# Performance work log

Measured on AMD Instinct MI355X. Metric: run time of the kernel, lower is better.

## Reference

```python
import jax, jax.numpy as jnp
import numpy as np

N_NODES = 50000
N_EDGES = 800000
IN_C = 64
OUT_C = 64
K = 4  # spectral coefficients; weight has K+1 slices (selfconn)
EPS = 1e-16  # PyG segment-softmax epsilon


def setup_inputs() -> dict:
    key = jax.random.key(0)
    k1, k2, k3, k4, k5 = jax.random.split(key, 5)
    x = jax.random.normal(k1, (N_NODES, IN_C), dtype=jnp.float32)
    edge_index = jax.random.randint(k2, (2, N_EDGES), 0, N_NODES, dtype=jnp.int64)
    edge_attr = jax.random.normal(k3, (N_EDGES, K), dtype=jnp.float32)
    # glorot-style scale for weight [K+1, in, out]
    stdv = np.sqrt(6.0 / (IN_C + OUT_C))
    weight = jax.random.uniform(k4, (K + 1, IN_C, OUT_C), dtype=jnp.float32,
                                minval=-stdv, maxval=stdv)
    bias = jnp.zeros((OUT_C,), dtype=jnp.float32)
    att_vector = jax.random.normal(k5, (IN_C, 1), dtype=jnp.float32) * 0.1
    return {"x": x, "edge_attr": edge_attr, "weight": weight, "bias": bias,
            "att_vector": att_vector, "edge_index": edge_index}


def _segment_softmax(logits, seg, num_segments):
    mx = jax.ops.segment_max(logits, seg, num_segments=num_segments)
    ex = jnp.exp(logits - mx[seg])
    den = jax.ops.segment_sum(ex, seg, num_segments=num_segments)
    return ex / (den[seg] + EPS)


def reference(x, edge_attr, weight, bias, att_vector, edge_index):
    src, dst = edge_index[0], edge_index[1]
    n_nodes = x.shape[0]
    # messages for all K coefficients at once: [E, K, C]
    msgs = edge_attr[:, :, None] * x[src][:, None, :]
    # sum branch: per-k scatter_add then per-k weight -> fused einsum
    sum_agg = jax.ops.segment_sum(msgs, dst, num_segments=n_nodes)  # [N, K, C]
    sum_out = x @ weight[-1] + jnp.einsum('nkc,kco->no', sum_agg, weight[:K])
    # attention branch
    pooled = msgs.mean(axis=1)                       # [E, C]
    raw_att = (pooled @ att_vector)[:, 0]            # [E]
    att_scores = _segment_softmax(raw_att, dst, n_nodes)
    att_agg = jax.ops.segment_sum(att_scores[:, None, None] * msgs, dst,
                                  num_segments=n_nodes)  # [N, K, C]
    out = sum_out + jnp.einsum('nkc,kco->no', att_agg, weight[:K]) + bias
    return out, att_scores
```

## Files before the change

kernel.cpp:

```cpp
#include <hip/hip_runtime.h>
#include <math.h>

#define C 64
#define KCOEF 4
#define FN 128
#define FK 64
#define APAD 65

#define BSH 6
#define RN 64
#define CAP 1280
#define EPB 4
#define MAXNBK 1024

__global__ __launch_bounds__(256) void kAH(const float* __restrict__ x,
        const float* __restrict__ attv, const int* __restrict__ dst,
        float* __restrict__ dvec, int* __restrict__ deg, int N, int E, int NBD) {
    if ((int)blockIdx.x < NBD) {
        int t = threadIdx.x;
        int n = blockIdx.x * 16 + (t >> 4);
        int q = t & 15;
        if (n >= N) return;
        float4 xv = *(const float4*)(x + (size_t)n * C + q * 4);
        float4 av = *(const float4*)(attv + q * 4);
        float p = xv.x * av.x + xv.y * av.y + xv.z * av.z + xv.w * av.w;
        #pragma unroll
        for (int o = 8; o > 0; o >>= 1) p += __shfl_xor(p, o, 16);
        if (q == 0) dvec[n] = p;
    } else {
        int e = ((int)blockIdx.x - NBD) * 256 + (int)threadIdx.x;
        if (e >= E) return;
        atomicAdd(&deg[dst[e]], 1);
    }
}

__global__ __launch_bounds__(256) void kS1(const int* __restrict__ deg,
        int* __restrict__ off, int* __restrict__ bsum, int N) {
    int g = blockIdx.x * 256 + threadIdx.x;
    int lane = threadIdx.x & 63, w = threadIdx.x >> 6;
    int v = (g < N) ? deg[g] : 0;
    int incl = v;
    #pragma unroll
    for (int s = 1; s < 64; s <<= 1) {
        int t = __shfl_up(incl, s);
        if (lane >= s) incl += t;
    }
    __shared__ int wtot[4];
    if (lane == 63) wtot[w] = incl;
    __syncthreads();
    int add = 0;
    for (int ww = 0; ww < w; ++ww) add += wtot[ww];
    int excl = incl - v + add;
    if (g < N) off[g] = excl;
    if (threadIdx.x == 255) bsum[blockIdx.x] = excl + v;
}

__global__ __launch_bounds__(256) void kS2(int* __restrict__ bsum, int NB) {
    int t = threadIdx.x;
    int lane = t & 63, w = t >> 6;
    int v = (t < NB) ? bsum[t] : 0;
    int incl = v;
    #pragma unroll
    for (int s = 1; s < 64; s <<= 1) {
        int tt = __shfl_up(incl, s);
        if (lane >= s) incl += tt;
    }
    __shared__ int wtot[4];
    if (lane == 63) wtot[w] = incl;
    __syncthreads();
    int add = 0;
    for (int ww = 0; ww < w; ++ww) add += wtot[ww];
    if (t < NB) bsum[t] = incl - v + add;
}

__global__ __launch_bounds__(256) void kS3(int* __restrict__ off,
        const int* __restrict__ bsum, int* __restrict__ gcur, int N, int E) {
    int g = blockIdx.x * 256 + threadIdx.x;
    if (g == 0) off[N] = E;
    if (g >= N) return;
    int o = off[g] + bsum[blockIdx.x];
    off[g] = o;
    if ((g & (RN - 1)) == 0) gcur[g >> BSH] = o;
}

__global__ __launch_bounds__(1024) void kBIN(const int* __restrict__ src,
        const int* __restrict__ dst, const float* __restrict__ ea,
        const float* __restrict__ dvec, int* __restrict__ gcur,
        float4* __restrict__ pay, int E, int NBK) {
    __shared__ int hist[MAXNBK];
    __shared__ int cursor[MAXNBK];
    int tid = threadIdx.x;
    int base = blockIdx.x * (1024 * EPB);
    for (int b = tid; b < NBK; b += 1024) hist[b] = 0;
    __syncthreads();
    #pragma unroll
    for (int i = 0; i < EPB; ++i) {
        int e = base + i * 1024 + tid;
        if (e < E) atomicAdd(&hist[dst[e] >> BSH], 1);
    }
    __syncthreads();
    for (int b = tid; b < NBK; b += 1024) cursor[b] = atomicAdd(&gcur[b], hist[b]);
    __syncthreads();
    #pragma unroll
    for (int i = 0; i < EPB; ++i) {
        int e = base + i * 1024 + tid;
        if (e < E) {
            int sN = src[e];
            int d  = dst[e];
            float4 a = ((const float4*)ea)[e];
            float mean = (a.x + a.y + a.z + a.w) * 0.25f;
            float r = mean * dvec[sN];
            int p = atomicAdd(&cursor[d >> BSH], 1);
            int xo = ((d & (RN - 1)) << 24) | (sN << 8);
            float4 q0 = make_float4(r, __int_as_float(xo), a.x, a.y);
            float4 q1 = make_float4(a.z, a.w, 0.f, 0.f);
            pay[(size_t)p * 2]     = q0;
            pay[(size_t)p * 2 + 1] = q1;
        }
    }
}

__global__ __launch_bounds__(512) void kAGG(const float* __restrict__ x,
        const float4* __restrict__ pay, const int* __restrict__ off,
        float* __restrict__ mA, float* __restrict__ invA,
        float* __restrict__ agg, int N) {
    __shared__ float  rA[CAP];
    __shared__ int    xoA[CAP];
    __shared__ float4 qA[CAP];
    __shared__ int    no[RN + 1];
    __shared__ int    ncur[RN];
    __shared__ float  mL[RN], ivL[RN];
    int tid = threadIdx.x;
    int n0 = (int)blockIdx.x << BSH;
    int n1 = min(n0 + RN, N);
    int nn = n1 - n0;
    int bstart = off[n0];
    int cnt = off[n1] - bstart;
    if (cnt > CAP) cnt = CAP;
    if (tid <= nn) {
        int o = off[n0 + tid] - bstart;
        o = min(o, CAP);
        no[tid] = o;
        if (tid < nn) ncur[tid] = o;
    }
    __syncthreads();
    for (int i = tid; i < cnt; i += 512) {
        float4 p0 = pay[(size_t)(bstart + i) * 2];
        float4 p1 = pay[(size_t)(bstart + i) * 2 + 1];
        int v = __float_as_int(p0.y);
        int p = atomicAdd(&ncur[v >> 24], 1);
        rA[p]  = p0.x;
        xoA[p] = v;
        qA[p]  = make_float4(p0.z, p0.w, p1.x, p1.y);
    }
    __syncthreads();
    int wv = tid >> 6, lane = tid & 63;
    for (int nl = wv; nl < nn; nl += 8) {
        int s = no[nl];
        int d = no[nl + 1] - s;
        int n = n0 + nl;
        if (d == 0) {
            if (lane == 0) { mL[nl] = 0.f; ivL[nl] = 1.f; mA[n] = 0.f; invA[n] = 1.f; }
            continue;
        }
        float m = -INFINITY;
        for (int i = lane; i < d; i += 64) m = fmaxf(m, rA[s + i]);
        #pragma unroll
        for (int o = 32; o > 0; o >>= 1) m = fmaxf(m, __shfl_xor(m, o));
        float ss = 0.f;
        for (int i = lane; i < d; i += 64) ss += expf(rA[s + i] - m);
        #pragma unroll
        for (int o = 32; o > 0; o >>= 1) ss += __shfl_xor(ss, o);
        float inv = 1.f / (ss + 1e-16f);
        if (lane == 0) { mL[nl] = m; ivL[nl] = inv; mA[n] = m; invA[n] = inv; }
    }
    __syncthreads();
    for (int i = tid; i < cnt; i += 512) {
        int dl = xoA[i] >> 24;
        rA[i] = 1.f + expf(rA[i] - mL[dl]) * ivL[dl];
    }
    __syncthreads();
    const char* xb = (const char*)x + (size_t)lane * 4;
    for (int nl = wv; nl < nn; nl += 8) {
        int s = no[nl];
        int d = no[nl + 1] - s;
        int n = n0 + nl;
        size_t ab = (size_t)n * (KCOEF * C) + lane;
        float a0 = 0.f, a1 = 0.f, a2 = 0.f, a3 = 0.f;
        #pragma unroll 4
        for (int j = 0; j < d; ++j) {
            float w = rA[s + j];
            float4 q = qA[s + j];
            int ob = xoA[s + j] & 0xFFFFFF;
            float xr = *(const float*)(xb + ob);
            float wx = w * xr;
            a0 = fmaf(q.x, wx, a0);
            a1 = fmaf(q.y, wx, a1);
            a2 = fmaf(q.z, wx, a2);
            a3 = fmaf(q.w, wx, a3);
        }
        agg[ab] = a0; agg[ab + 64] = a1; agg[ab + 128] = a2; agg[ab + 192] = a3;
    }
}

__global__ __launch_bounds__(256) void kF3(const float* __restrict__ agg,
        const float* __restrict__ x, const float* __restrict__ W,
        const float* __restrict__ bias, float* __restrict__ out_node, int N) {
    __shared__ float As[FN][APAD];
    __shared__ float Ws[FK][C];
    int tid = threadIdx.x;
    int nbase = blockIdx.x * FN;
    int ng = tid >> 3;
    int cg = tid & 7;
    float4 acc0[4], acc1[4];
    #pragma unroll
    for (int j = 0; j < 4; ++j) { acc0[j] = {0,0,0,0}; acc1[j] = {0,0,0,0}; }

    int srow_q = tid & 15;
    int srow_b = tid >> 4;

    for (int k0 = 0; k0 < 320; k0 += FK) {
        #pragma unroll
        for (int pass = 0; pass < 8; ++pass) {
            int row = pass * 16 + srow_b;
            int n = nbase + row; if (n >= N) n = N - 1;
            float4 v;
            if (k0 < 256) v = *(const float4*)(agg + (size_t)n * 256 + k0 + srow_q * 4);
            else          v = *(const float4*)(x   + (size_t)n * C   + srow_q * 4);
            As[row][srow_q * 4 + 0] = v.x;
            As[row][srow_q * 4 + 1] = v.y;
            As[row][srow_q * 4 + 2] = v.z;
            As[row][srow_q * 4 + 3] = v.w;
        }
        #pragma unroll
        for (int p = 0; p < 4; ++p) {
            int idx = tid + p * 256;
            ((float4*)Ws)[idx] = ((const float4*)(W + (size_t)k0 * C))[idx];
        }
        __syncthreads();
        #pragma unroll 2
        for (int i = 0; i < FK; ++i) {
            float a0 = As[ng * 4 + 0][i];
            float a1 = As[ng * 4 + 1][i];
            float a2 = As[ng * 4 + 2][i];
            float a3 = As[ng * 4 + 3][i];
            float4 w0 = *(const float4*)&Ws[i][cg * 8];
            float4 w1 = *(const float4*)&Ws[i][cg * 8 + 4];
            acc0[0].x = fmaf(a0, w0.x, acc0[0].x); acc0[0].y = fmaf(a0, w0.y, acc0[0].y);
            acc0[0].z = fmaf(a0, w0.z, acc0[0].z); acc0[0].w = fmaf(a0, w0.w, acc0[0].w);
            acc1[0].x = fmaf(a0, w1.x, acc1[0].x); acc1[0].y = fmaf(a0, w1.y, acc1[0].y);
            acc1[0].z = fmaf(a0, w1.z, acc1[0].z); acc1[0].w = fmaf(a0, w1.w, acc1[0].w);
            acc0[1].x = fmaf(a1, w0.x, acc0[1].x); acc0[1].y = fmaf(a1, w0.y, acc0[1].y);
            acc0[1].z = fmaf(a1, w0.z, acc0[1].z); acc0[1].w = fmaf(a1, w0.w, acc0[1].w);
            acc1[1].x = fmaf(a1, w1.x, acc1[1].x); acc1[1].y = fmaf(a1, w1.y, acc1[1].y);
            acc1[1].z = fmaf(a1, w1.z, acc1[1].z); acc1[1].w = fmaf(a1, w1.w, acc1[1].w);
            acc0[2].x = fmaf(a2, w0.x, acc0[2].x); acc0[2].y = fmaf(a2, w0.y, acc0[2].y);
            acc0[2].z = fmaf(a2, w0.z, acc0[2].z); acc0[2].w = fmaf(a2, w0.w, acc0[2].w);
            acc1[2].x = fmaf(a2, w1.x, acc1[2].x); acc1[2].y = fmaf(a2, w1.y, acc1[2].y);
            acc1[2].z = fmaf(a2, w1.z, acc1[2].z); acc1[2].w = fmaf(a2, w1.w, acc1[2].w);
            acc0[3].x = fmaf(a3, w0.x, acc0[3].x); acc0[3].y = fmaf(a3, w0.y, acc0[3].y);
            acc0[3].z = fmaf(a3, w0.z, acc0[3].z); acc0[3].w = fmaf(a3, w0.w, acc0[3].w);
            acc1[3].x = fmaf(a3, w1.x, acc1[3].x); acc1[3].y = fmaf(a3, w1.y, acc1[3].y);
            acc1[3].z = fmaf(a3, w1.z, acc1[3].z); acc1[3].w = fmaf(a3, w1.w, acc1[3].w);
        }
        __syncthreads();
    }
    float4 bA = *(const float4*)(bias + cg * 8);
    float4 bB = *(const float4*)(bias + cg * 8 + 4);
    #pragma unroll
    for (int j = 0; j < 4; ++j) {
        int n = nbase + ng * 4 + j;
        if (n < N) {
            float4 oA = { acc0[j].x + bA.x, acc0[j].y + bA.y, acc0[j].z + bA.z, acc0[j].w + bA.w };
            float4 oB = { acc1[j].x + bB.x, acc1[j].y + bB.y, acc1[j].z + bB.z, acc1[j].w + bB.w };
            *(float4*)(out_node + (size_t)n * C + cg * 8)     = oA;
            *(float4*)(out_node + (size_t)n * C + cg * 8 + 4) = oB;
        }
    }
}

__global__ __launch_bounds__(256) void kT(const int* __restrict__ src,
        const int* __restrict__ dst, const float* __restrict__ ea,
        const float* __restrict__ dvec, const float* __restrict__ mA,
        const float* __restrict__ invA, float* __restrict__ out_att, int E) {
    int e = blockIdx.x * 256 + threadIdx.x;
    if (e >= E) return;
    float4 a = ((const float4*)ea)[e];
    float mean = (a.x + a.y + a.z + a.w) * 0.25f;
    float r = mean * dvec[src[e]];
    int d = dst[e];
    out_att[e] = expf(r - mA[d]) * invA[d];
}

extern "C" void kernel_launch(void* const* d_in, const int* in_sizes, int n_in,
                              void* d_out, int out_size, void* d_ws, size_t ws_size,
                              hipStream_t stream) {
    const float* x    = (const float*)d_in[0];
    const float* ea   = (const float*)d_in[1];
    const float* W    = (const float*)d_in[2];
    const float* bias = (const float*)d_in[3];
    const float* attv = (const float*)d_in[4];
    const int*   ei   = (const int*)d_in[5];

    int N = in_sizes[0] / C;
    int E = in_sizes[5] / 2;
    const int* src = ei;
    const int* dst = ei + E;

    float* out_node = (float*)d_out;
    float* out_att  = (float*)d_out + (size_t)N * C;

    char* ws = (char*)d_ws;
    float* agg  = (float*)ws; ws += (size_t)N * KCOEF * C * sizeof(float);
    float4* pay = (float4*)ws; ws += (size_t)E * 32;
    float* dvec = (float*)ws; ws += (size_t)N * sizeof(float);
    int*   deg  = (int*)ws;   ws += (size_t)N * sizeof(int);
    int*   off  = (int*)ws;   ws += (size_t)(N + 1) * sizeof(int);
    float* mA   = (float*)ws; ws += (size_t)N * sizeof(float);
    int*   gcur = (int*)ws;   ws += MAXNBK * sizeof(int);
    int*   bsum = (int*)ws;   ws += 1024;

    float* invA = (float*)deg;

    int NB  = (N + 255) / 256;
    int NBD = (N + 15) / 16;
    int NBH = (E + 255) / 256;
    int NBK = (N + RN - 1) >> BSH;
    int NBB = (E + 1024 * EPB - 1) / (1024 * EPB);
    int NBF = (N + FN - 1) / FN;

    hipMemsetAsync(deg, 0, (size_t)N * sizeof(int), stream);
    kAH  <<<NBD + NBH, 256, 0, stream>>>(x, attv, dst, dvec, deg, N, E, NBD);
    kS1  <<<NB, 256, 0, stream>>>(deg, off, bsum, N);
    kS2  <<<1, 256, 0, stream>>>(bsum, NB);
    kS3  <<<NB, 256, 0, stream>>>(off, bsum, gcur, N, E);
    kBIN <<<NBB, 1024, 0, stream>>>(src, dst, ea, dvec, gcur, pay, E, NBK);
    kAGG <<<NBK, 512, 0, stream>>>(x, pay, off, mA, invA, agg, N);
    kF3  <<<NBF, 256, 0, stream>>>(agg, x, W, bias, out_node, N);
    kT   <<<NBH, 256, 0, stream>>>(src, dst, ea, dvec, mA, invA, out_att, E);
}
```

Baseline: 252.0 us.

## Replace per-node degree scan with per-bucket histogram and in-block node offsets

The per-node degree atomics and the three-kernel prefix scan over N nodes are replaced by a shared-memory histogram per 64-node bucket and a single-block scan over about 800 buckets. Per-node offsets inside each bucket are now rebuilt in the aggregation kernel by counting a new byte array of local destination indices and doing a wave scan. The payload is also split into a 16-byte record and an 8-byte record instead of a padded 32-byte one, which cuts write and read traffic. This removes two launches and the global per-node atomics, but adds a counting pass and an extra byte stream inside kAGG.

```diff
diff --git a/kernel.cpp b/kernel.cpp
--- a/kernel.cpp
+++ b/kernel.cpp
@@ -11,11 +11,13 @@
 #define RN 64
 #define CAP 1280
 #define EPB 4
+#define EH  16
 #define MAXNBK 1024
 
 __global__ __launch_bounds__(256) void kAH(const float* __restrict__ x,
         const float* __restrict__ attv, const int* __restrict__ dst,
-        float* __restrict__ dvec, int* __restrict__ deg, int N, int E, int NBD) {
+        float* __restrict__ dvec, int* __restrict__ bcnt,
+        int N, int E, int NBD, int NBK) {
     if ((int)blockIdx.x < NBD) {
         int t = threadIdx.x;
         int n = blockIdx.x * 16 + (t >> 4);
@@ -28,65 +30,48 @@
         for (int o = 8; o > 0; o >>= 1) p += __shfl_xor(p, o, 16);
         if (q == 0) dvec[n] = p;
     } else {
-        int e = ((int)blockIdx.x - NBD) * 256 + (int)threadIdx.x;
-        if (e >= E) return;
-        atomicAdd(&deg[dst[e]], 1);
-    }
-}
-
-__global__ __launch_bounds__(256) void kS1(const int* __restrict__ deg,
-        int* __restrict__ off, int* __restrict__ bsum, int N) {
-    int g = blockIdx.x * 256 + threadIdx.x;
-    int lane = threadIdx.x & 63, w = threadIdx.x >> 6;
-    int v = (g < N) ? deg[g] : 0;
-    int incl = v;
-    #pragma unroll
-    for (int s = 1; s < 64; s <<= 1) {
-        int t = __shfl_up(incl, s);
-        if (lane >= s) incl += t;
-    }
-    __shared__ int wtot[4];
-    if (lane == 63) wtot[w] = incl;
-    __syncthreads();
-    int add = 0;
-    for (int ww = 0; ww < w; ++ww) add += wtot[ww];
-    int excl = incl - v + add;
-    if (g < N) off[g] = excl;
-    if (threadIdx.x == 255) bsum[blockIdx.x] = excl + v;
-}
-
-__global__ __launch_bounds__(256) void kS2(int* __restrict__ bsum, int NB) {
-    int t = threadIdx.x;
-    int lane = t & 63, w = t >> 6;
-    int v = (t < NB) ? bsum[t] : 0;
+        __shared__ int hist[MAXNBK];
+        int tid = threadIdx.x;
+        for (int b = tid; b < NBK; b += 256) hist[b] = 0;
+        __syncthreads();
+        int base = ((int)blockIdx.x - NBD) * (256 * EH);
+        for (int i = 0; i < EH; ++i) {
+            int e = base + i * 256 + tid;
+            if (e < E) atomicAdd(&hist[dst[e] >> BSH], 1);
+        }
+        __syncthreads();
+        for (int b = tid; b < NBK; b += 256) {
+            int h = hist[b];
+            if (h) atomicAdd(&bcnt[b], h);
+        }
+    }
+}
+
+__global__ __launch_bounds__(1024) void kSB(const int* __restrict__ bcnt,
+        int* __restrict__ base_, int* __restrict__ gcur, int NBK) {
+    int t = threadIdx.x, lane = t & 63, wv = t >> 6;
+    int v = (t < NBK) ? bcnt[t] : 0;
     int incl = v;
     #pragma unroll
     for (int s = 1; s < 64; s <<= 1) {
         int tt = __shfl_up(incl, s);
         if (lane >= s) incl += tt;
     }
-    __shared__ int wtot[4];
-    if (lane == 63) wtot[w] = incl;
+    __shared__ int wtot[16];
+    if (lane == 63) wtot[wv] = incl;
     __syncthreads();
     int add = 0;
-    for (int ww = 0; ww < w; ++ww) add += wtot[ww];
-    if (t < NB) bsum[t] = incl - v + add;
-}
-
-__global__ __launch_bounds__(256) void kS3(int* __restrict__ off,
-        const int* __restrict__ bsum, int* __restrict__ gcur, int N, int E) {
-    int g = blockIdx.x * 256 + threadIdx.x;
-    if (g == 0) off[N] = E;
-    if (g >= N) return;
-    int o = off[g] + bsum[blockIdx.x];
-    off[g] = o;
-    if ((g & (RN - 1)) == 0) gcur[g >> BSH] = o;
+    for (int w = 0; w < wv; ++w) add += wtot[w];
+    int excl = incl - v + add;
+    if (t <= NBK) base_[t] = excl;
+    if (t <  NBK) gcur[t]  = excl;
 }
 
 __global__ __launch_bounds__(1024) void kBIN(const int* __restrict__ src,
         const int* __restrict__ dst, const float* __restrict__ ea,
         const float* __restrict__ dvec, int* __restrict__ gcur,
-        float4* __restrict__ pay, int E, int NBK) {
+        float4* __restrict__ pay16, float2* __restrict__ pay8,
+        unsigned char* __restrict__ dlA, int E, int NBK) {
     __shared__ int hist[MAXNBK];
     __shared__ int cursor[MAXNBK];
     int tid = threadIdx.x;
@@ -99,7 +84,10 @@
         if (e < E) atomicAdd(&hist[dst[e] >> BSH], 1);
     }
     __syncthreads();
-    for (int b = tid; b < NBK; b += 1024) cursor[b] = atomicAdd(&gcur[b], hist[b]);
+    for (int b = tid; b < NBK; b += 1024) {
+        int h = hist[b];
+        cursor[b] = h ? atomicAdd(&gcur[b], h) : 0;
+    }
     __syncthreads();
     #pragma unroll
     for (int i = 0; i < EPB; ++i) {
@@ -110,18 +98,19 @@
             float4 a = ((const float4*)ea)[e];
             float mean = (a.x + a.y + a.z + a.w) * 0.25f;
             float r = mean * dvec[sN];
+            int dl = d & (RN - 1);
             int p = atomicAdd(&cursor[d >> BSH], 1);
-            int xo = ((d & (RN - 1)) << 24) | (sN << 8);
-            float4 q0 = make_float4(r, __int_as_float(xo), a.x, a.y);
-            float4 q1 = make_float4(a.z, a.w, 0.f, 0.f);
-            pay[(size_t)p * 2]     = q0;
-            pay[(size_t)p * 2 + 1] = q1;
+            int xo = (dl << 24) | (sN << 8);
+            pay16[p] = make_float4(r, __int_as_float(xo), a.x, a.y);
+            pay8[p]  = make_float2(a.z, a.w);
+            dlA[p]   = (unsigned char)dl;
         }
     }
 }
 
 __global__ __launch_bounds__(512) void kAGG(const float* __restrict__ x,
-        const float4* __restrict__ pay, const int* __restrict__ off,
+        const float4* __restrict__ pay16, const float2* __restrict__ pay8,
+        const unsigned char* __restrict__ dlA, const int* __restrict__ base_,
         float* __restrict__ mA, float* __restrict__ invA,
         float* __restrict__ agg, int N) {
     __shared__ float  rA[CAP];
@@ -129,24 +118,38 @@
     __shared__ float4 qA[CAP];
     __shared__ int    no[RN + 1];
     __shared__ int    ncur[RN];
+    __shared__ int    ncnt[RN];
     __shared__ float  mL[RN], ivL[RN];
     int tid = threadIdx.x;
-    int n0 = (int)blockIdx.x << BSH;
+    int b = (int)blockIdx.x;
+    int n0 = b << BSH;
     int n1 = min(n0 + RN, N);
     int nn = n1 - n0;
-    int bstart = off[n0];
-    int cnt = off[n1] - bstart;
+    int bstart = base_[b];
+    int cnt = base_[b + 1] - bstart;
     if (cnt > CAP) cnt = CAP;
-    if (tid <= nn) {
-        int o = off[n0 + tid] - bstart;
-        o = min(o, CAP);
-        no[tid] = o;
-        if (tid < nn) ncur[tid] = o;
-    }
+    if (tid < RN) ncnt[tid] = 0;
+    __syncthreads();
+    for (int i = tid; i < cnt; i += 512) atomicAdd(&ncnt[dlA[bstart + i]], 1);
+    __syncthreads();
+    int wv = tid >> 6, lane = tid & 63;
+    if (wv == 0) {
+        int v = (lane < nn) ? ncnt[lane] : 0;
+        int incl = v;
+        #pragma unroll
+        for (int s = 1; s < 64; s <<= 1) {
+            int tt = __shfl_up(incl, s);
+            if (lane >= s) incl += tt;
+        }
+        no[lane + 1] = incl;
+        if (lane == 0) no[0] = 0;
+    }
+    __syncthreads();
+    if (tid < nn) ncur[tid] = no[tid];
     __syncthreads();
     for (int i = tid; i < cnt; i += 512) {
-        float4 p0 = pay[(size_t)(bstart + i) * 2];
-        float4 p1 = pay[(size_t)(bstart + i) * 2 + 1];
+        float4 p0 = pay16[(size_t)bstart + i];
+        float2 p1 = pay8[(size_t)bstart + i];
         int v = __float_as_int(p0.y);
         int p = atomicAdd(&ncur[v >> 24], 1);
         rA[p]  = p0.x;
@@ -154,7 +157,6 @@
         qA[p]  = make_float4(p0.z, p0.w, p1.x, p1.y);
     }
     __syncthreads();
-    int wv = tid >> 6, lane = tid & 63;
     for (int nl = wv; nl < nn; nl += 8) {
         int s = no[nl];
         int d = no[nl + 1] - s;
@@ -311,31 +313,30 @@
     float* out_att  = (float*)d_out + (size_t)N * C;
 
     char* ws = (char*)d_ws;
-    float* agg  = (float*)ws; ws += (size_t)N * KCOEF * C * sizeof(float);
-    float4* pay = (float4*)ws; ws += (size_t)E * 32;
+    float* agg   = (float*)ws; ws += (size_t)N * KCOEF * C * sizeof(float);
+    float4* pay16 = (float4*)ws; ws += (size_t)E * 16;
+    float2* pay8  = (float2*)ws; ws += (size_t)E * 8;
+    unsigned char* dlA = (unsigned char*)ws; ws += (size_t)E;
+    ws = (char*)(((size_t)ws + 255) & ~(size_t)255);
     float* dvec = (float*)ws; ws += (size_t)N * sizeof(float);
-    int*   deg  = (int*)ws;   ws += (size_t)N * sizeof(int);
-    int*   off  = (int*)ws;   ws += (size_t)(N + 1) * sizeof(int);
     float* mA   = (float*)ws; ws += (size_t)N * sizeof(float);
+    float* invA = (float*)ws; ws += (size_t)N * sizeof(float);
+    int*   bcnt = (int*)ws;   ws += MAXNBK * sizeof(int);
+    int*   base_= (int*)ws;   ws += (MAXNBK + 1) * sizeof(int);
     int*   gcur = (int*)ws;   ws += MAXNBK * sizeof(int);
-    int*   bsum = (int*)ws;   ws += 1024;
-
-    float* invA = (float*)deg;
-
-    int NB  = (N + 255) / 256;
-    int NBD = (N + 15) / 16;
-    int NBH = (E + 255) / 256;
-    int NBK = (N + RN - 1) >> BSH;
-    int NBB = (E + 1024 * EPB - 1) / (1024 * EPB);
-    int NBF = (N + FN - 1) / FN;
-
-    hipMemsetAsync(deg, 0, (size_t)N * sizeof(int), stream);
-    kAH  <<<NBD + NBH, 256, 0, stream>>>(x, attv, dst, dvec, deg, N, E, NBD);
-    kS1  <<<NB, 256, 0, stream>>>(deg, off, bsum, N);
-    kS2  <<<1, 256, 0, stream>>>(bsum, NB);
-    kS3  <<<NB, 256, 0, stream>>>(off, bsum, gcur, N, E);
-    kBIN <<<NBB, 1024, 0, stream>>>(src, dst, ea, dvec, gcur, pay, E, NBK);
-    kAGG <<<NBK, 512, 0, stream>>>(x, pay, off, mA, invA, agg, N);
+
+    int NBD  = (N + 15) / 16;
+    int NBH2 = (E + 256 * EH - 1) / (256 * EH);
+    int NBK  = (N + RN - 1) >> BSH;
+    int NBB  = (E + 1024 * EPB - 1) / (1024 * EPB);
+    int NBF  = (N + FN - 1) / FN;
+    int NBT  = (E + 255) / 256;
+
+    hipMemsetAsync(bcnt, 0, MAXNBK * sizeof(int), stream);
+    kAH  <<<NBD + NBH2, 256, 0, stream>>>(x, attv, dst, dvec, bcnt, N, E, NBD, NBK);
+    kSB  <<<1, 1024, 0, stream>>>(bcnt, base_, gcur, NBK);
+    kBIN <<<NBB, 1024, 0, stream>>>(src, dst, ea, dvec, gcur, pay16, pay8, dlA, E, NBK);
+    kAGG <<<NBK, 512, 0, stream>>>(x, pay16, pay8, dlA, base_, mA, invA, agg, N);
     kF3  <<<NBF, 256, 0, stream>>>(agg, x, W, bias, out_node, N);
-    kT   <<<NBH, 256, 0, stream>>>(src, dst, ea, dvec, mA, invA, out_att, E);
-}
+    kT   <<<NBT, 256, 0, stream>>>(src, dst, ea, dvec, mA, invA, out_att, E);
+}
```

New measurement: 238.8 us. 1.06x faster.
